# Performance work log

Measured on AMD Instinct MI355X. Metric: run time of the kernel, lower is better.

## Reference

```python
import jax, jax.numpy as jnp
import numpy as np

D_MODEL = 768
N_HEADS = 12
D_K = D_MODEL // N_HEADS
NEG = -1e9


def setup_inputs() -> dict:
    key = jax.random.key(0)
    ks = jax.random.split(key, 10)
    B, S = 2, 2048
    x = jax.random.normal(ks[0], (B, S, D_MODEL), dtype=jnp.float32)
    # causal mask, broadcastable over batch and heads
    mask = jnp.tril(jnp.ones((S, S), dtype=jnp.int32))[None, None]
    scale = 1.0 / np.sqrt(D_MODEL)
    def lin(k):
        return jax.random.normal(k, (D_MODEL, D_MODEL), dtype=jnp.float32) * scale
    return {
        "x": x, "mask": mask,
        "wq": lin(ks[1]), "bq": jnp.zeros((D_MODEL,), jnp.float32),
        "wk": lin(ks[2]), "bk": jnp.zeros((D_MODEL,), jnp.float32),
        "wv": lin(ks[3]), "bv": jnp.zeros((D_MODEL,), jnp.float32),
        "wo": lin(ks[4]), "bo": jnp.zeros((D_MODEL,), jnp.float32),
    }


def reference(x, mask, wq, bq, wk, bk, wv, bv, wo, bo):
    B, S, _ = x.shape
    def split_heads(t):  # [B,S,D] -> [B,H,S,dk]
        return t.reshape(B, S, N_HEADS, D_K).transpose(0, 2, 1, 3)
    q = split_heads(x @ wq + bq)
    k = split_heads(x @ wk + bk)
    v = split_heads(x @ wv + bv)
    scores = jnp.einsum("bhqd,bhkd->bhqk", q, k) / jnp.sqrt(jnp.float32(D_K))
    scores = jnp.where(mask == 0, NEG, scores)
    attn = jax.nn.softmax(scores, axis=-1)
    # dropout is identity in eval mode
    ctx = jnp.einsum("bhqk,bhkd->bhqd", attn, v)
    ctx = ctx.transpose(0, 2, 1, 3).reshape(B, S, D_MODEL)
    return ctx @ wo + bo
```

## Files before the change

### kernel.cpp

```cpp
#include <hip/hip_runtime.h>
#include <hip/hip_bf16.h>
#include <stdint.h>

#define DM   768
#define NH   12
#define DKH  64
#define BB   2
#define SS   2048
#define MT   (BB*SS)
#define NQKV (3*DM)

typedef __attribute__((ext_vector_type(8))) short short8;
typedef __attribute__((ext_vector_type(4))) float f32x4;

__device__ __forceinline__ unsigned short f2bf(float f) {
    union { float f; unsigned u; } v; v.f = f;
    unsigned r = v.u + 0x7fffu + ((v.u >> 16) & 1u);
    return (unsigned short)(r >> 16);
}

__device__ __forceinline__ void gload_lds16(const unsigned short* g, unsigned short* l) {
    __builtin_amdgcn_global_load_lds((const __attribute__((address_space(1))) void*)g,
                                     (__attribute__((address_space(3))) void*)l, 16, 0, 0);
}

__global__ void k_conv_x(const float* __restrict__ x, unsigned short* __restrict__ xb) {
    int i = blockIdx.x * 256 + threadIdx.x;
    const float4 v = ((const float4*)x)[i];
    ushort4 o;
    o.x = f2bf(v.x); o.y = f2bf(v.y); o.z = f2bf(v.z); o.w = f2bf(v.w);
    ((ushort4*)xb)[i] = o;
}

__global__ void k_conv_w(const float* __restrict__ wq, const float* __restrict__ wk,
                         const float* __restrict__ wv, const float* __restrict__ wo,
                         unsigned short* __restrict__ wT) {
    int idx = blockIdx.x * 256 + threadIdx.x;
    int r = idx / DM;
    int k = idx - r * DM;
    int sel = r / DM;
    int n = r - sel * DM;
    const float* w = (sel == 0) ? wq : (sel == 1) ? wk : (sel == 2) ? wv : wo;
    wT[idx] = f2bf(w[k * DM + n]);
}

__launch_bounds__(256)
__global__ void k_gemm_qkv(const unsigned short* __restrict__ xb,
                           const unsigned short* __restrict__ wT,
                           const float* __restrict__ bq, const float* __restrict__ bk,
                           const float* __restrict__ bv,
                           unsigned short* __restrict__ Qb,
                           unsigned short* __restrict__ Kb,
                           unsigned short* __restrict__ Vt) {
    __shared__ __align__(16) unsigned short As[128][32];
    __shared__ __align__(16) unsigned short Bs[128][32];
    const int t = threadIdx.x;
    const int m0 = blockIdx.x * 128;
    const int n0 = blockIdx.y * 128;
    const int wid = t >> 6, lane = t & 63, q4 = lane >> 4, l16 = lane & 15;
    const int wm = (wid >> 1) * 64, wn = (wid & 1) * 64;

    const int srow = wid * 32 + (lane >> 2);
    const int koff = (lane & 3) * 8;
    const unsigned short* AgL = xb + (size_t)(m0 + srow) * DM + koff;
    const unsigned short* AgH = AgL + (size_t)16 * DM;
    const unsigned short* BgL = wT + (size_t)(n0 + srow) * DM + koff;
    const unsigned short* BgH = BgL + (size_t)16 * DM;
    unsigned short* ldsA1 = &As[wid*32][0];
    unsigned short* ldsA2 = &As[wid*32 + 16][0];
    unsigned short* ldsB1 = &Bs[wid*32][0];
    unsigned short* ldsB2 = &Bs[wid*32 + 16][0];

    f32x4 acc[4][4];
    for (int i = 0; i < 4; i++) for (int j = 0; j < 4; j++)
        acc[i][j] = (f32x4){0.f, 0.f, 0.f, 0.f};

    for (int kt = 0; kt < DM; kt += 32) {
        gload_lds16(AgL + kt, ldsA1);
        gload_lds16(AgH + kt, ldsA2);
        gload_lds16(BgL + kt, ldsB1);
        gload_lds16(BgH + kt, ldsB2);
        __syncthreads();
        short8 af[4], bf[4];
        for (int i = 0; i < 4; i++) af[i] = *(const short8*)&As[wm + i*16 + l16][q4*8];
        for (int i = 0; i < 4; i++) bf[i] = *(const short8*)&Bs[wn + i*16 + l16][q4*8];
        for (int mi = 0; mi < 4; mi++)
            for (int ni = 0; ni < 4; ni++)
                acc[mi][ni] = __builtin_amdgcn_mfma_f32_16x16x32_bf16(af[mi], bf[ni], acc[mi][ni], 0, 0, 0);
        __syncthreads();
    }

    const int sel = n0 / DM;
    const float* bias = (sel == 0) ? bq : (sel == 1) ? bk : bv;
    for (int ni = 0; ni < 4; ni++) {
        const int col = n0 + wn + ni*16 + l16;
        const int c = col - sel * DM;
        const float bsv = bias[c];
        const int h = c >> 6, d = c & 63;
        for (int mi = 0; mi < 4; mi++) {
            for (int r = 0; r < 4; r++) {
                const int row = m0 + wm + mi*16 + q4*4 + r;
                const int b = row >> 11, s = row & 2047;
                const int bh = b * NH + h;
                float v = acc[mi][ni][r] + bsv;
                if (sel == 0) {
                    Qb[(bh*SS + s)*DKH + d] = f2bf(v * 0.125f);
                } else if (sel == 1) {
                    Kb[(bh*SS + s)*DKH + d] = f2bf(v);
                } else {
                    Vt[(bh*DKH + d)*SS + s] = f2bf(v);
                }
            }
        }
    }
}

__launch_bounds__(256)
__global__ void k_attn(const unsigned short* __restrict__ Qb,
                       const unsigned short* __restrict__ Kb,
                       const unsigned short* __restrict__ Vt,
                       unsigned short* __restrict__ ctx) {
    __shared__ __align__(16) unsigned short Ks[2][64][72];
    __shared__ __align__(16) unsigned short Vs[2][64][72];
    __shared__ __align__(16) unsigned short P[4][16][72];
    const int t = threadIdx.x;
    const int wid = t >> 6, lane = t & 63, q4 = lane >> 4, l16 = lane & 15;
    const int lin = blockIdx.x;
    const int bh = lin % (BB * NH);
    const int pair = lin / (BB * NH);
    const int b = bh / NH, h = bh - b * NH;

    const unsigned short* Qp = Qb + (size_t)bh * SS * DKH;
    const unsigned short* Kp = Kb + (size_t)bh * SS * DKH;
    const unsigned short* Vp = Vt + (size_t)bh * DKH * SS;

    const int srow = t >> 3;
    const int scol = (t & 7) * 8;

    for (int it = 0; it < 2; it++) {
        const int qblk = it ? (31 - pair) : pair;
        const int qw = qblk * 64 + wid * 16;

        short8 qf[2];
        for (int kc = 0; kc < 2; kc++)
            qf[kc] = *(const short8*)(Qp + (qw + l16)*DKH + kc*32 + q4*8);

        f32x4 accO[4];
        for (int j = 0; j < 4; j++) accO[j] = (f32x4){0.f, 0.f, 0.f, 0.f};
        float lacc[4] = {0.f, 0.f, 0.f, 0.f};

        {
            uint4 k0 = *(const uint4*)(Kp + (size_t)(srow)      * DKH + scol);
            uint4 k1 = *(const uint4*)(Kp + (size_t)(srow + 32) * DKH + scol);
            uint4 v0 = *(const uint4*)(Vp + (size_t)(srow)      * SS  + scol);
            uint4 v1 = *(const uint4*)(Vp + (size_t)(srow + 32) * SS  + scol);
            *(uint4*)&Ks[0][srow][scol]      = k0;
            *(uint4*)&Ks[0][srow + 32][scol] = k1;
            *(uint4*)&Vs[0][srow][scol]      = v0;
            *(uint4*)&Vs[0][srow + 32][scol] = v1;
        }
        __syncthreads();

        for (int kt = 0; kt <= qblk; kt++) {
            const int cb = kt & 1, nb = cb ^ 1;
            const bool hasN = (kt < qblk);
            uint4 nk0, nk1, nv0, nv1;
            if (hasN) {
                const int kn = (kt + 1) * 64;
                nk0 = *(const uint4*)(Kp + (size_t)(kn + srow)      * DKH + scol);
                nk1 = *(const uint4*)(Kp + (size_t)(kn + srow + 32) * DKH + scol);
                nv0 = *(const uint4*)(Vp + (size_t)(srow)      * SS + kn + scol);
                nv1 = *(const uint4*)(Vp + (size_t)(srow + 32) * SS + kn + scol);
            }
            short8 kf[4][2];
            #pragma unroll
            for (int ni = 0; ni < 4; ni++)
                #pragma unroll
                for (int kc = 0; kc < 2; kc++)
                    kf[ni][kc] = *(const short8*)&Ks[cb][ni*16 + l16][kc*32 + q4*8];
            f32x4 S[4];
            #pragma unroll
            for (int j = 0; j < 4; j++) S[j] = (f32x4){0.f, 0.f, 0.f, 0.f};
            #pragma unroll
            for (int ni = 0; ni < 4; ni++) {
                S[ni] = __builtin_amdgcn_mfma_f32_16x16x32_bf16(qf[0], kf[ni][0], S[ni], 0, 0, 0);
                S[ni] = __builtin_amdgcn_mfma_f32_16x16x32_bf16(qf[1], kf[ni][1], S[ni], 0, 0, 0);
            }
            if (kt == qblk) {
                #pragma unroll
                for (int ni = 0; ni < 4; ni++) {
                    const int key = kt*64 + ni*16 + l16;
                    #pragma unroll
                    for (int r = 0; r < 4; r++) {
                        const int qrow = qw + q4*4 + r;
                        float p = (key > qrow) ? 0.f : __expf(S[ni][r]);
                        lacc[r] += p;
                        P[wid][q4*4 + r][ni*16 + l16] = f2bf(p);
                    }
                }
            } else {
                #pragma unroll
                for (int ni = 0; ni < 4; ni++)
                    #pragma unroll
                    for (int r = 0; r < 4; r++) {
                        float p = __expf(S[ni][r]);
                        lacc[r] += p;
                        P[wid][q4*4 + r][ni*16 + l16] = f2bf(p);
                    }
            }
            asm volatile("s_waitcnt lgkmcnt(0)" ::: "memory");
            short8 pf[2];
            #pragma unroll
            for (int kc = 0; kc < 2; kc++)
                pf[kc] = *(const short8*)&P[wid][l16][kc*32 + q4*8];
            short8 vf[4][2];
            #pragma unroll
            for (int ndi = 0; ndi < 4; ndi++)
                #pragma unroll
                for (int kc = 0; kc < 2; kc++)
                    vf[ndi][kc] = *(const short8*)&Vs[cb][ndi*16 + l16][kc*32 + q4*8];
            #pragma unroll
            for (int ndi = 0; ndi < 4; ndi++)
                #pragma unroll
                for (int kc = 0; kc < 2; kc++)
                    accO[ndi] = __builtin_amdgcn_mfma_f32_16x16x32_bf16(pf[kc], vf[ndi][kc], accO[ndi], 0, 0, 0);
            if (hasN) {
                *(uint4*)&Ks[nb][srow][scol]      = nk0;
                *(uint4*)&Ks[nb][srow + 32][scol] = nk1;
                *(uint4*)&Vs[nb][srow][scol]      = nv0;
                *(uint4*)&Vs[nb][srow + 32][scol] = nv1;
            }
            __syncthreads();
        }

        for (int r = 0; r < 4; r++) {
            float l = lacc[r];
            for (int off = 1; off < 16; off <<= 1) l += __shfl_xor(l, off);
            const float inv = 1.0f / l;
            const int s = qw + q4*4 + r;
            for (int ni = 0; ni < 4; ni++)
                ctx[((size_t)(b*SS + s))*DM + h*64 + ni*16 + l16] = f2bf(accO[ni][r] * inv);
        }
    }
}

__launch_bounds__(256)
__global__ void k_gemm_proj(const unsigned short* __restrict__ ctx,
                            const unsigned short* __restrict__ woT,
                            const float* __restrict__ bo,
                            float* __restrict__ out) {
    __shared__ __align__(16) unsigned short As[128][32];
    __shared__ __align__(16) unsigned short Bs[64][32];
    const int t = threadIdx.x;
    const int m0 = blockIdx.x * 128;
    const int n0 = blockIdx.y * 64;
    const int wid = t >> 6, lane = t & 63, q4 = lane >> 4, l16 = lane & 15;
    const int wm = (wid >> 1) * 64, wn = (wid & 1) * 32;

    const int srowA = wid * 32 + (lane >> 2);
    const int srowB = wid * 16 + (lane >> 2);
    const int koff = (lane & 3) * 8;
    const unsigned short* AgL = ctx + (size_t)(m0 + srowA) * DM + koff;
    const unsigned short* AgH = AgL + (size_t)16 * DM;
    const unsigned short* BgL = woT + (size_t)(n0 + srowB) * DM + koff;
    unsigned short* ldsA1 = &As[wid*32][0];
    unsigned short* ldsA2 = &As[wid*32 + 16][0];
    unsigned short* ldsB1 = &Bs[wid*16][0];

    f32x4 acc[4][2];
    for (int i = 0; i < 4; i++) for (int j = 0; j < 2; j++)
        acc[i][j] = (f32x4){0.f, 0.f, 0.f, 0.f};

    for (int kt = 0; kt < DM; kt += 32) {
        gload_lds16(AgL + kt, ldsA1);
        gload_lds16(AgH + kt, ldsA2);
        gload_lds16(BgL + kt, ldsB1);
        __syncthreads();
        short8 af[4], bf[2];
        for (int i = 0; i < 4; i++) af[i] = *(const short8*)&As[wm + i*16 + l16][q4*8];
        for (int i = 0; i < 2; i++) bf[i] = *(const short8*)&Bs[wn + i*16 + l16][q4*8];
        for (int mi = 0; mi < 4; mi++)
            for (int ni = 0; ni < 2; ni++)
                acc[mi][ni] = __builtin_amdgcn_mfma_f32_16x16x32_bf16(af[mi], bf[ni], acc[mi][ni], 0, 0, 0);
        __syncthreads();
    }

    for (int ni = 0; ni < 2; ni++) {
        const int col = n0 + wn + ni*16 + l16;
        const float bsv = bo[col];
        for (int mi = 0; mi < 4; mi++) {
            for (int r = 0; r < 4; r++) {
                const int row = m0 + wm + mi*16 + q4*4 + r;
                out[(size_t)row * DM + col] = acc[mi][ni][r] + bsv;
            }
        }
    }
}

extern "C" void kernel_launch(void* const* d_in, const int* in_sizes, int n_in,
                              void* d_out, int out_size, void* d_ws, size_t ws_size,
                              hipStream_t stream) {
    const float* x  = (const float*)d_in[0];
    const float* wq = (const float*)d_in[2];
    const float* bq = (const float*)d_in[3];
    const float* wk = (const float*)d_in[4];
    const float* bk = (const float*)d_in[5];
    const float* wv = (const float*)d_in[6];
    const float* bv = (const float*)d_in[7];
    const float* wo = (const float*)d_in[8];
    const float* bo = (const float*)d_in[9];
    float* out = (float*)d_out;

    unsigned short* xb  = (unsigned short*)d_ws;
    unsigned short* wT  = xb + (size_t)MT * DM;
    unsigned short* Qb  = wT + (size_t)4 * DM * DM;
    unsigned short* Kb  = Qb + (size_t)BB * NH * SS * DKH;
    unsigned short* Vt  = Kb + (size_t)BB * NH * SS * DKH;
    unsigned short* ctx = Vt + (size_t)BB * NH * SS * DKH;

    k_conv_x<<<(MT * DM / 4) / 256, 256, 0, stream>>>(x, xb);
    k_conv_w<<<(4 * DM * DM) / 256, 256, 0, stream>>>(wq, wk, wv, wo, wT);
    dim3 g1(MT / 128, NQKV / 128);
    k_gemm_qkv<<<g1, 256, 0, stream>>>(xb, wT, bq, bk, bv, Qb, Kb, Vt);
    k_attn<<<dim3(16 * BB * NH), 256, 0, stream>>>(Qb, Kb, Vt, ctx);
    dim3 g3(MT / 128, DM / 64);
    k_gemm_proj<<<g3, 256, 0, stream>>>(ctx, wT + (size_t)3 * DM * DM, bo, out);
}
```

Measured before the change: 194.4 us.

## Tile weight transpose through LDS and restructure attention to 2 waves per q-block

The weight conversion kernel now transposes 32x32 tiles through shared memory, so both its reads and its writes are coalesced instead of strided. The attention kernel switches from 4 waves handling a paired q-block (16 rows each) to 2 waves handling one 64-row q-block (32 rows each), launched as one block per q-block with heaviest blocks scheduled first. Each K/V fragment read from LDS now feeds twice as many MFMAs, and P conversion uses packed bf16x2 intrinsics. The diagonal tile also skips the fully masked half for wave 0. The trade-offs are fewer waves per block and more blocks, plus load imbalance from launching causal-length blocks individually rather than in balanced pairs.

After: 226.3 us. 16.4% more time.

```diff
diff --git a/kernel.cpp b/kernel.cpp
--- a/kernel.cpp
+++ b/kernel.cpp
@@ -35,13 +35,18 @@
 __global__ void k_conv_w(const float* __restrict__ wq, const float* __restrict__ wk,
                          const float* __restrict__ wv, const float* __restrict__ wo,
                          unsigned short* __restrict__ wT) {
-    int idx = blockIdx.x * 256 + threadIdx.x;
-    int r = idx / DM;
-    int k = idx - r * DM;
-    int sel = r / DM;
-    int n = r - sel * DM;
+    __shared__ float tile[32][33];
+    const int sel = blockIdx.z;
     const float* w = (sel == 0) ? wq : (sel == 1) ? wk : (sel == 2) ? wv : wo;
-    wT[idx] = f2bf(w[k * DM + n]);
+    const int k0 = blockIdx.x * 32, n0 = blockIdx.y * 32;
+    const int tx = threadIdx.x, ty = threadIdx.y;
+    #pragma unroll
+    for (int j = 0; j < 4; j++)
+        tile[ty + 8*j][tx] = w[(size_t)(k0 + ty + 8*j) * DM + n0 + tx];
+    __syncthreads();
+    #pragma unroll
+    for (int j = 0; j < 4; j++)
+        wT[(size_t)(sel*DM + n0 + ty + 8*j) * DM + k0 + tx] = f2bf(tile[tx][ty + 8*j]);
 }
 
 __launch_bounds__(256)
@@ -115,131 +120,166 @@
     }
 }
 
-__launch_bounds__(256)
+__launch_bounds__(128)
 __global__ void k_attn(const unsigned short* __restrict__ Qb,
                        const unsigned short* __restrict__ Kb,
                        const unsigned short* __restrict__ Vt,
                        unsigned short* __restrict__ ctx) {
     __shared__ __align__(16) unsigned short Ks[2][64][72];
     __shared__ __align__(16) unsigned short Vs[2][64][72];
-    __shared__ __align__(16) unsigned short P[4][16][72];
+    __shared__ __align__(16) unsigned short P[2][32][68];
     const int t = threadIdx.x;
     const int wid = t >> 6, lane = t & 63, q4 = lane >> 4, l16 = lane & 15;
     const int lin = blockIdx.x;
     const int bh = lin % (BB * NH);
-    const int pair = lin / (BB * NH);
+    const int qblk = 31 - lin / (BB * NH);
     const int b = bh / NH, h = bh - b * NH;
+    const int qw = qblk * 64 + wid * 32;
 
     const unsigned short* Qp = Qb + (size_t)bh * SS * DKH;
     const unsigned short* Kp = Kb + (size_t)bh * SS * DKH;
     const unsigned short* Vp = Vt + (size_t)bh * DKH * SS;
 
-    const int srow = t >> 3;
-    const int scol = (t & 7) * 8;
-
-    for (int it = 0; it < 2; it++) {
-        const int qblk = it ? (31 - pair) : pair;
-        const int qw = qblk * 64 + wid * 16;
-
-        short8 qf[2];
+    short8 qf[2][2];
+    for (int mi = 0; mi < 2; mi++)
         for (int kc = 0; kc < 2; kc++)
-            qf[kc] = *(const short8*)(Qp + (qw + l16)*DKH + kc*32 + q4*8);
-
-        f32x4 accO[4];
-        for (int j = 0; j < 4; j++) accO[j] = (f32x4){0.f, 0.f, 0.f, 0.f};
-        float lacc[4] = {0.f, 0.f, 0.f, 0.f};
-
-        {
-            uint4 k0 = *(const uint4*)(Kp + (size_t)(srow)      * DKH + scol);
-            uint4 k1 = *(const uint4*)(Kp + (size_t)(srow + 32) * DKH + scol);
-            uint4 v0 = *(const uint4*)(Vp + (size_t)(srow)      * SS  + scol);
-            uint4 v1 = *(const uint4*)(Vp + (size_t)(srow + 32) * SS  + scol);
-            *(uint4*)&Ks[0][srow][scol]      = k0;
-            *(uint4*)&Ks[0][srow + 32][scol] = k1;
-            *(uint4*)&Vs[0][srow][scol]      = v0;
-            *(uint4*)&Vs[0][srow + 32][scol] = v1;
-        }
-        __syncthreads();
-
-        for (int kt = 0; kt <= qblk; kt++) {
-            const int cb = kt & 1, nb = cb ^ 1;
-            const bool hasN = (kt < qblk);
-            uint4 nk0, nk1, nv0, nv1;
-            if (hasN) {
-                const int kn = (kt + 1) * 64;
-                nk0 = *(const uint4*)(Kp + (size_t)(kn + srow)      * DKH + scol);
-                nk1 = *(const uint4*)(Kp + (size_t)(kn + srow + 32) * DKH + scol);
-                nv0 = *(const uint4*)(Vp + (size_t)(srow)      * SS + kn + scol);
-                nv1 = *(const uint4*)(Vp + (size_t)(srow + 32) * SS + kn + scol);
-            }
-            short8 kf[4][2];
-            #pragma unroll
-            for (int ni = 0; ni < 4; ni++)
-                #pragma unroll
-                for (int kc = 0; kc < 2; kc++)
-                    kf[ni][kc] = *(const short8*)&Ks[cb][ni*16 + l16][kc*32 + q4*8];
-            f32x4 S[4];
-            #pragma unroll
-            for (int j = 0; j < 4; j++) S[j] = (f32x4){0.f, 0.f, 0.f, 0.f};
-            #pragma unroll
-            for (int ni = 0; ni < 4; ni++) {
-                S[ni] = __builtin_amdgcn_mfma_f32_16x16x32_bf16(qf[0], kf[ni][0], S[ni], 0, 0, 0);
-                S[ni] = __builtin_amdgcn_mfma_f32_16x16x32_bf16(qf[1], kf[ni][1], S[ni], 0, 0, 0);
-            }
-            if (kt == qblk) {
+            qf[mi][kc] = *(const short8*)(Qp + (qw + mi*16 + l16)*DKH + kc*32 + q4*8);
+
+    f32x4 accO[2][4];
+    for (int i = 0; i < 2; i++) for (int j = 0; j < 4; j++)
+        accO[i][j] = (f32x4){0.f, 0.f, 0.f, 0.f};
+    float lacc[2][4];
+    for (int i = 0; i < 2; i++) for (int r = 0; r < 4; r++) lacc[i][r] = 0.f;
+
+    const int sr = t >> 3;
+    const int sc = (t & 7) * 8;
+
+    #pragma unroll
+    for (int j = 0; j < 4; j++) {
+        uint4 kv = *(const uint4*)(Kp + (size_t)(sr + 16*j) * DKH + sc);
+        uint4 vv = *(const uint4*)(Vp + (size_t)(sr + 16*j) * SS + sc);
+        *(uint4*)&Ks[0][sr + 16*j][sc] = kv;
+        *(uint4*)&Vs[0][sr + 16*j][sc] = vv;
+    }
+    __syncthreads();
+
+    for (int kt = 0; kt <= qblk; kt++) {
+        const int cb = kt & 1, nb = cb ^ 1;
+        const bool hasN = (kt < qblk);
+        uint4 nk[4], nv[4];
+        if (hasN) {
+            const int kn = (kt + 1) * 64;
+            #pragma unroll
+            for (int j = 0; j < 4; j++) {
+                nk[j] = *(const uint4*)(Kp + (size_t)(kn + sr + 16*j) * DKH + sc);
+                nv[j] = *(const uint4*)(Vp + (size_t)(sr + 16*j) * SS + kn + sc);
+            }
+        }
+        short8 kf[4][2];
+        #pragma unroll
+        for (int ni = 0; ni < 4; ni++)
+            #pragma unroll
+            for (int kc = 0; kc < 2; kc++)
+                kf[ni][kc] = *(const short8*)&Ks[cb][ni*16 + l16][kc*32 + q4*8];
+        f32x4 S[2][4];
+        #pragma unroll
+        for (int i = 0; i < 2; i++)
+            #pragma unroll
+            for (int j = 0; j < 4; j++)
+                S[i][j] = (f32x4){0.f, 0.f, 0.f, 0.f};
+        #pragma unroll
+        for (int ni = 0; ni < 4; ni++)
+            #pragma unroll
+            for (int mi = 0; mi < 2; mi++) {
+                S[mi][ni] = __builtin_amdgcn_mfma_f32_16x16x32_bf16(qf[mi][0], kf[ni][0], S[mi][ni], 0, 0, 0);
+                S[mi][ni] = __builtin_amdgcn_mfma_f32_16x16x32_bf16(qf[mi][1], kf[ni][1], S[mi][ni], 0, 0, 0);
+            }
+        if (kt == qblk) {
+            #pragma unroll
+            for (int mi = 0; mi < 2; mi++)
                 #pragma unroll
                 for (int ni = 0; ni < 4; ni++) {
-                    const int key = kt*64 + ni*16 + l16;
+                    const int pr = mi*16 + q4*4, pc = ni*16 + l16;
+                    if (wid == 0 && ni >= 2) {
+                        P[wid][pr+0][pc] = 0; P[wid][pr+1][pc] = 0;
+                        P[wid][pr+2][pc] = 0; P[wid][pr+3][pc] = 0;
+                        continue;
+                    }
+                    const int key = qblk*64 + ni*16 + l16;
+                    float p[4];
                     #pragma unroll
                     for (int r = 0; r < 4; r++) {
-                        const int qrow = qw + q4*4 + r;
-                        float p = (key > qrow) ? 0.f : __expf(S[ni][r]);
-                        lacc[r] += p;
-                        P[wid][q4*4 + r][ni*16 + l16] = f2bf(p);
+                        const int qrow = qw + mi*16 + q4*4 + r;
+                        p[r] = (key > qrow) ? 0.f : __expf(S[mi][ni][r]);
+                        lacc[mi][r] += p[r];
                     }
+                    union { __hip_bfloat162 v; unsigned u; } u01, u23;
+                    u01.v = __float22bfloat162_rn(make_float2(p[0], p[1]));
+                    u23.v = __float22bfloat162_rn(make_float2(p[2], p[3]));
+                    P[wid][pr+0][pc] = (unsigned short)(u01.u & 0xffffu);
+                    P[wid][pr+1][pc] = (unsigned short)(u01.u >> 16);
+                    P[wid][pr+2][pc] = (unsigned short)(u23.u & 0xffffu);
+                    P[wid][pr+3][pc] = (unsigned short)(u23.u >> 16);
                 }
-            } else {
+        } else {
+            #pragma unroll
+            for (int mi = 0; mi < 2; mi++)
                 #pragma unroll
-                for (int ni = 0; ni < 4; ni++)
+                for (int ni = 0; ni < 4; ni++) {
+                    float p[4];
                     #pragma unroll
                     for (int r = 0; r < 4; r++) {
-                        float p = __expf(S[ni][r]);
-                        lacc[r] += p;
-                        P[wid][q4*4 + r][ni*16 + l16] = f2bf(p);
+                        p[r] = __expf(S[mi][ni][r]);
+                        lacc[mi][r] += p[r];
                     }
-            }
-            asm volatile("s_waitcnt lgkmcnt(0)" ::: "memory");
-            short8 pf[2];
+                    union { __hip_bfloat162 v; unsigned u; } u01, u23;
+                    u01.v = __float22bfloat162_rn(make_float2(p[0], p[1]));
+                    u23.v = __float22bfloat162_rn(make_float2(p[2], p[3]));
+                    const int pr = mi*16 + q4*4, pc = ni*16 + l16;
+                    P[wid][pr+0][pc] = (unsigned short)(u01.u & 0xffffu);
+                    P[wid][pr+1][pc] = (unsigned short)(u01.u >> 16);
+                    P[wid][pr+2][pc] = (unsigned short)(u23.u & 0xffffu);
+                    P[wid][pr+3][pc] = (unsigned short)(u23.u >> 16);
+                }
+        }
+        asm volatile("s_waitcnt lgkmcnt(0)" ::: "memory");
+        short8 pf[2][2];
+        #pragma unroll
+        for (int mi = 0; mi < 2; mi++)
             #pragma unroll
             for (int kc = 0; kc < 2; kc++)
-                pf[kc] = *(const short8*)&P[wid][l16][kc*32 + q4*8];
-            short8 vf[4][2];
-            #pragma unroll
-            for (int ndi = 0; ndi < 4; ndi++)
+                pf[mi][kc] = *(const short8*)&P[wid][mi*16 + l16][kc*32 + q4*8];
+        short8 vf[4][2];
+        #pragma unroll
+        for (int ndi = 0; ndi < 4; ndi++)
+            #pragma unroll
+            for (int kc = 0; kc < 2; kc++)
+                vf[ndi][kc] = *(const short8*)&Vs[cb][ndi*16 + l16][kc*32 + q4*8];
+        #pragma unroll
+        for (int ndi = 0; ndi < 4; ndi++)
+            #pragma unroll
+            for (int kc = 0; kc < 2; kc++)
                 #pragma unroll
-                for (int kc = 0; kc < 2; kc++)
-                    vf[ndi][kc] = *(const short8*)&Vs[cb][ndi*16 + l16][kc*32 + q4*8];
-            #pragma unroll
-            for (int ndi = 0; ndi < 4; ndi++)
-                #pragma unroll
-                for (int kc = 0; kc < 2; kc++)
-                    accO[ndi] = __builtin_amdgcn_mfma_f32_16x16x32_bf16(pf[kc], vf[ndi][kc], accO[ndi], 0, 0, 0);
-            if (hasN) {
-                *(uint4*)&Ks[nb][srow][scol]      = nk0;
-                *(uint4*)&Ks[nb][srow + 32][scol] = nk1;
-                *(uint4*)&Vs[nb][srow][scol]      = nv0;
-                *(uint4*)&Vs[nb][srow + 32][scol] = nv1;
-            }
-            __syncthreads();
-        }
-
+                for (int mi = 0; mi < 2; mi++)
+                    accO[mi][ndi] = __builtin_amdgcn_mfma_f32_16x16x32_bf16(pf[mi][kc], vf[ndi][kc], accO[mi][ndi], 0, 0, 0);
+        if (hasN) {
+            #pragma unroll
+            for (int j = 0; j < 4; j++) {
+                *(uint4*)&Ks[nb][sr + 16*j][sc] = nk[j];
+                *(uint4*)&Vs[nb][sr + 16*j][sc] = nv[j];
+            }
+        }
+        __syncthreads();
+    }
+
+    for (int mi = 0; mi < 2; mi++) {
         for (int r = 0; r < 4; r++) {
-            float l = lacc[r];
+            float l = lacc[mi][r];
             for (int off = 1; off < 16; off <<= 1) l += __shfl_xor(l, off);
             const float inv = 1.0f / l;
-            const int s = qw + q4*4 + r;
+            const int s = qw + mi*16 + q4*4 + r;
             for (int ni = 0; ni < 4; ni++)
-                ctx[((size_t)(b*SS + s))*DM + h*64 + ni*16 + l16] = f2bf(accO[ni][r] * inv);
+                ctx[((size_t)(b*SS + s))*DM + h*64 + ni*16 + l16] = f2bf(accO[mi][ni][r] * inv);
         }
     }
 }
@@ -319,10 +359,10 @@
     unsigned short* ctx = Vt + (size_t)BB * NH * SS * DKH;
 
     k_conv_x<<<(MT * DM / 4) / 256, 256, 0, stream>>>(x, xb);
-    k_conv_w<<<(4 * DM * DM) / 256, 256, 0, stream>>>(wq, wk, wv, wo, wT);
+    k_conv_w<<<dim3(DM/32, DM/32, 4), dim3(32, 8), 0, stream>>>(wq, wk, wv, wo, wT);
     dim3 g1(MT / 128, NQKV / 128);
     k_gemm_qkv<<<g1, 256, 0, stream>>>(xb, wT, bq, bk, bv, Qb, Kb, Vt);
-    k_attn<<<dim3(16 * BB * NH), 256, 0, stream>>>(Qb, Kb, Vt, ctx);
+    k_attn<<<dim3(32 * BB * NH), 128, 0, stream>>>(Qb, Kb, Vt, ctx);
     dim3 g3(MT / 128, DM / 64);
     k_gemm_proj<<<g3, 256, 0, stream>>>(ctx, wT + (size_t)3 * DM * DM, bo, out);
 }
```

## Tile weight transpose through LDS, split attention into one q-block per workgroup

Applied to the files above, without the earlier changes.

The weight conversion kernel now transposes through a padded 32x33 LDS tile, so both the global reads and the global writes are coalesced. The attention kernel no longer pairs two q-blocks per workgroup. It launches one workgroup per q-block, longest blocks first, which doubles the grid size and helps balance the causal workload. On the diagonal tile, sub-tiles above the diagonal are now written as zeros without computing exp, and the P scratch padding shrinks to 68. bf16 packing now uses the hardware float2-to-bfloat2 conversion.

New measurement: 179.6 us. 7.6% less time.

```diff
diff --git a/kernel.cpp b/kernel.cpp
--- a/kernel.cpp
+++ b/kernel.cpp
@@ -35,13 +35,18 @@
 __global__ void k_conv_w(const float* __restrict__ wq, const float* __restrict__ wk,
                          const float* __restrict__ wv, const float* __restrict__ wo,
                          unsigned short* __restrict__ wT) {
-    int idx = blockIdx.x * 256 + threadIdx.x;
-    int r = idx / DM;
-    int k = idx - r * DM;
-    int sel = r / DM;
-    int n = r - sel * DM;
+    __shared__ float tile[32][33];
+    const int sel = blockIdx.z;
     const float* w = (sel == 0) ? wq : (sel == 1) ? wk : (sel == 2) ? wv : wo;
-    wT[idx] = f2bf(w[k * DM + n]);
+    const int k0 = blockIdx.x * 32, n0 = blockIdx.y * 32;
+    const int tx = threadIdx.x, ty = threadIdx.y;
+    #pragma unroll
+    for (int j = 0; j < 4; j++)
+        tile[ty + 8*j][tx] = w[(size_t)(k0 + ty + 8*j) * DM + n0 + tx];
+    __syncthreads();
+    #pragma unroll
+    for (int j = 0; j < 4; j++)
+        wT[(size_t)(sel*DM + n0 + ty + 8*j) * DM + k0 + tx] = f2bf(tile[tx][ty + 8*j]);
 }
 
 __launch_bounds__(256)
@@ -122,125 +127,151 @@
                        unsigned short* __restrict__ ctx) {
     __shared__ __align__(16) unsigned short Ks[2][64][72];
     __shared__ __align__(16) unsigned short Vs[2][64][72];
-    __shared__ __align__(16) unsigned short P[4][16][72];
+    __shared__ __align__(16) unsigned short P[4][16][68];
     const int t = threadIdx.x;
     const int wid = t >> 6, lane = t & 63, q4 = lane >> 4, l16 = lane & 15;
     const int lin = blockIdx.x;
     const int bh = lin % (BB * NH);
-    const int pair = lin / (BB * NH);
+    const int qblk = 31 - lin / (BB * NH);
     const int b = bh / NH, h = bh - b * NH;
+    const int qw = qblk * 64 + wid * 16;
 
     const unsigned short* Qp = Qb + (size_t)bh * SS * DKH;
     const unsigned short* Kp = Kb + (size_t)bh * SS * DKH;
     const unsigned short* Vp = Vt + (size_t)bh * DKH * SS;
 
-    const int srow = t >> 3;
-    const int scol = (t & 7) * 8;
-
-    for (int it = 0; it < 2; it++) {
-        const int qblk = it ? (31 - pair) : pair;
-        const int qw = qblk * 64 + wid * 16;
-
-        short8 qf[2];
-        for (int kc = 0; kc < 2; kc++)
-            qf[kc] = *(const short8*)(Qp + (qw + l16)*DKH + kc*32 + q4*8);
-
-        f32x4 accO[4];
-        for (int j = 0; j < 4; j++) accO[j] = (f32x4){0.f, 0.f, 0.f, 0.f};
-        float lacc[4] = {0.f, 0.f, 0.f, 0.f};
-
-        {
-            uint4 k0 = *(const uint4*)(Kp + (size_t)(srow)      * DKH + scol);
-            uint4 k1 = *(const uint4*)(Kp + (size_t)(srow + 32) * DKH + scol);
-            uint4 v0 = *(const uint4*)(Vp + (size_t)(srow)      * SS  + scol);
-            uint4 v1 = *(const uint4*)(Vp + (size_t)(srow + 32) * SS  + scol);
-            *(uint4*)&Ks[0][srow][scol]      = k0;
-            *(uint4*)&Ks[0][srow + 32][scol] = k1;
-            *(uint4*)&Vs[0][srow][scol]      = v0;
-            *(uint4*)&Vs[0][srow + 32][scol] = v1;
-        }
-        __syncthreads();
-
-        for (int kt = 0; kt <= qblk; kt++) {
-            const int cb = kt & 1, nb = cb ^ 1;
-            const bool hasN = (kt < qblk);
-            uint4 nk0, nk1, nv0, nv1;
-            if (hasN) {
-                const int kn = (kt + 1) * 64;
-                nk0 = *(const uint4*)(Kp + (size_t)(kn + srow)      * DKH + scol);
-                nk1 = *(const uint4*)(Kp + (size_t)(kn + srow + 32) * DKH + scol);
-                nv0 = *(const uint4*)(Vp + (size_t)(srow)      * SS + kn + scol);
-                nv1 = *(const uint4*)(Vp + (size_t)(srow + 32) * SS + kn + scol);
-            }
-            short8 kf[4][2];
-            #pragma unroll
-            for (int ni = 0; ni < 4; ni++)
-                #pragma unroll
-                for (int kc = 0; kc < 2; kc++)
-                    kf[ni][kc] = *(const short8*)&Ks[cb][ni*16 + l16][kc*32 + q4*8];
-            f32x4 S[4];
-            #pragma unroll
-            for (int j = 0; j < 4; j++) S[j] = (f32x4){0.f, 0.f, 0.f, 0.f};
+    const int sr = t >> 3;
+    const int sc = (t & 7) * 8;
+
+    short8 qf[2];
+    for (int kc = 0; kc < 2; kc++)
+        qf[kc] = *(const short8*)(Qp + (qw + l16)*DKH + kc*32 + q4*8);
+
+    f32x4 accO[4];
+    for (int j = 0; j < 4; j++) accO[j] = (f32x4){0.f, 0.f, 0.f, 0.f};
+    float lacc[4] = {0.f, 0.f, 0.f, 0.f};
+
+    {
+        uint4 k0 = *(const uint4*)(Kp + (size_t)(sr)      * DKH + sc);
+        uint4 k1 = *(const uint4*)(Kp + (size_t)(sr + 32) * DKH + sc);
+        uint4 v0 = *(const uint4*)(Vp + (size_t)(sr)      * SS  + sc);
+        uint4 v1 = *(const uint4*)(Vp + (size_t)(sr + 32) * SS  + sc);
+        *(uint4*)&Ks[0][sr][sc]      = k0;
+        *(uint4*)&Ks[0][sr + 32][sc] = k1;
+        *(uint4*)&Vs[0][sr][sc]      = v0;
+        *(uint4*)&Vs[0][sr + 32][sc] = v1;
+    }
+    __syncthreads();
+
+    for (int kt = 0; kt <= qblk; kt++) {
+        const int cb = kt & 1, nb = cb ^ 1;
+        const bool hasN = (kt < qblk);
+        uint4 nk0, nk1, nv0, nv1;
+        if (hasN) {
+            const int kn = (kt + 1) * 64;
+            nk0 = *(const uint4*)(Kp + (size_t)(kn + sr)      * DKH + sc);
+            nk1 = *(const uint4*)(Kp + (size_t)(kn + sr + 32) * DKH + sc);
+            nv0 = *(const uint4*)(Vp + (size_t)(sr)      * SS + kn + sc);
+            nv1 = *(const uint4*)(Vp + (size_t)(sr + 32) * SS + kn + sc);
+        }
+        short8 kf[4][2];
+        #pragma unroll
+        for (int ni = 0; ni < 4; ni++)
+            #pragma unroll
+            for (int kc = 0; kc < 2; kc++)
+                kf[ni][kc] = *(const short8*)&Ks[cb][ni*16 + l16][kc*32 + q4*8];
+        f32x4 S[4];
+        #pragma unroll
+        for (int j = 0; j < 4; j++) S[j] = (f32x4){0.f, 0.f, 0.f, 0.f};
+        #pragma unroll
+        for (int ni = 0; ni < 4; ni++) {
+            S[ni] = __builtin_amdgcn_mfma_f32_16x16x32_bf16(qf[0], kf[ni][0], S[ni], 0, 0, 0);
+            S[ni] = __builtin_amdgcn_mfma_f32_16x16x32_bf16(qf[1], kf[ni][1], S[ni], 0, 0, 0);
+        }
+        if (kt == qblk) {
             #pragma unroll
             for (int ni = 0; ni < 4; ni++) {
-                S[ni] = __builtin_amdgcn_mfma_f32_16x16x32_bf16(qf[0], kf[ni][0], S[ni], 0, 0, 0);
-                S[ni] = __builtin_amdgcn_mfma_f32_16x16x32_bf16(qf[1], kf[ni][1], S[ni], 0, 0, 0);
-            }
-            if (kt == qblk) {
-                #pragma unroll
-                for (int ni = 0; ni < 4; ni++) {
-                    const int key = kt*64 + ni*16 + l16;
+                const int pr = q4*4, pc = ni*16 + l16;
+                if (ni > wid) {
+                    P[wid][pr+0][pc] = 0; P[wid][pr+1][pc] = 0;
+                    P[wid][pr+2][pc] = 0; P[wid][pr+3][pc] = 0;
+                    continue;
+                }
+                float p[4];
+                if (ni == wid) {
                     #pragma unroll
                     for (int r = 0; r < 4; r++) {
                         const int qrow = qw + q4*4 + r;
-                        float p = (key > qrow) ? 0.f : __expf(S[ni][r]);
-                        lacc[r] += p;
-                        P[wid][q4*4 + r][ni*16 + l16] = f2bf(p);
+                        const int key = qblk*64 + ni*16 + l16;
+                        p[r] = (key > qrow) ? 0.f : __expf(S[ni][r]);
+                        lacc[r] += p[r];
+                    }
+                } else {
+                    #pragma unroll
+                    for (int r = 0; r < 4; r++) {
+                        p[r] = __expf(S[ni][r]);
+                        lacc[r] += p[r];
                     }
                 }
-            } else {
+                union { __hip_bfloat162 v; unsigned u; } u01, u23;
+                u01.v = __float22bfloat162_rn(make_float2(p[0], p[1]));
+                u23.v = __float22bfloat162_rn(make_float2(p[2], p[3]));
+                P[wid][pr+0][pc] = (unsigned short)(u01.u & 0xffffu);
+                P[wid][pr+1][pc] = (unsigned short)(u01.u >> 16);
+                P[wid][pr+2][pc] = (unsigned short)(u23.u & 0xffffu);
+                P[wid][pr+3][pc] = (unsigned short)(u23.u >> 16);
+            }
+        } else {
+            #pragma unroll
+            for (int ni = 0; ni < 4; ni++) {
+                float p[4];
                 #pragma unroll
-                for (int ni = 0; ni < 4; ni++)
-                    #pragma unroll
-                    for (int r = 0; r < 4; r++) {
-                        float p = __expf(S[ni][r]);
-                        lacc[r] += p;
-                        P[wid][q4*4 + r][ni*16 + l16] = f2bf(p);
-                    }
+                for (int r = 0; r < 4; r++) {
+                    p[r] = __expf(S[ni][r]);
+                    lacc[r] += p[r];
+                }
+                union { __hip_bfloat162 v; unsigned u; } u01, u23;
+                u01.v = __float22bfloat162_rn(make_float2(p[0], p[1]));
+                u23.v = __float22bfloat162_rn(make_float2(p[2], p[3]));
+                const int pr = q4*4, pc = ni*16 + l16;
+                P[wid][pr+0][pc] = (unsigned short)(u01.u & 0xffffu);
+                P[wid][pr+1][pc] = (unsigned short)(u01.u >> 16);
+                P[wid][pr+2][pc] = (unsigned short)(u23.u & 0xffffu);
+                P[wid][pr+3][pc] = (unsigned short)(u23.u >> 16);
             }
-            asm volatile("s_waitcnt lgkmcnt(0)" ::: "memory");
-            short8 pf[2];
+        }
+        asm volatile("s_waitcnt lgkmcnt(0)" ::: "memory");
+        short8 pf[2];
+        #pragma unroll
+        for (int kc = 0; kc < 2; kc++)
+            pf[kc] = *(const short8*)&P[wid][l16][kc*32 + q4*8];
+        short8 vf[4][2];
+        #pragma unroll
+        for (int ndi = 0; ndi < 4; ndi++)
             #pragma unroll
             for (int kc = 0; kc < 2; kc++)
-                pf[kc] = *(const short8*)&P[wid][l16][kc*32 + q4*8];
-            short8 vf[4][2];
-            #pragma unroll
-            for (int ndi = 0; ndi < 4; ndi++)
-                #pragma unroll
-                for (int kc = 0; kc < 2; kc++)
-                    vf[ndi][kc] = *(const short8*)&Vs[cb][ndi*16 + l16][kc*32 + q4*8];
-            #pragma unroll
-            for (int ndi = 0; ndi < 4; ndi++)
-                #pragma unroll
-                for (int kc = 0; kc < 2; kc++)
-                    accO[ndi] = __builtin_amdgcn_mfma_f32_16x16x32_bf16(pf[kc], vf[ndi][kc], accO[ndi], 0, 0, 0);
-            if (hasN) {
-                *(uint4*)&Ks[nb][srow][scol]      = nk0;
-                *(uint4*)&Ks[nb][srow + 32][scol] = nk1;
-                *(uint4*)&Vs[nb][srow][scol]      = nv0;
-                *(uint4*)&Vs[nb][srow + 32][scol] = nv1;
-            }
-            __syncthreads();
-        }
-
-        for (int r = 0; r < 4; r++) {
-            float l = lacc[r];
-            for (int off = 1; off < 16; off <<= 1) l += __shfl_xor(l, off);
-            const float inv = 1.0f / l;
-            const int s = qw + q4*4 + r;
-            for (int ni = 0; ni < 4; ni++)
-                ctx[((size_t)(b*SS + s))*DM + h*64 + ni*16 + l16] = f2bf(accO[ni][r] * inv);
-        }
+                vf[ndi][kc] = *(const short8*)&Vs[cb][ndi*16 + l16][kc*32 + q4*8];
+        #pragma unroll
+        for (int ndi = 0; ndi < 4; ndi++)
+            #pragma unroll
+            for (int kc = 0; kc < 2; kc++)
+                accO[ndi] = __builtin_amdgcn_mfma_f32_16x16x32_bf16(pf[kc], vf[ndi][kc], accO[ndi], 0, 0, 0);
+        if (hasN) {
+            *(uint4*)&Ks[nb][sr][sc]      = nk0;
+            *(uint4*)&Ks[nb][sr + 32][sc] = nk1;
+            *(uint4*)&Vs[nb][sr][sc]      = nv0;
+            *(uint4*)&Vs[nb][sr + 32][sc] = nv1;
+        }
+        __syncthreads();
+    }
+
+    for (int r = 0; r < 4; r++) {
+        float l = lacc[r];
+        for (int off = 1; off < 16; off <<= 1) l += __shfl_xor(l, off);
+        const float inv = 1.0f / l;
+        const int s = qw + q4*4 + r;
+        for (int ni = 0; ni < 4; ni++)
+            ctx[((size_t)(b*SS + s))*DM + h*64 + ni*16 + l16] = f2bf(accO[ni][r] * inv);
     }
 }
 
@@ -319,10 +350,10 @@
     unsigned short* ctx = Vt + (size_t)BB * NH * SS * DKH;
 
     k_conv_x<<<(MT * DM / 4) / 256, 256, 0, stream>>>(x, xb);
-    k_conv_w<<<(4 * DM * DM) / 256, 256, 0, stream>>>(wq, wk, wv, wo, wT);
+    k_conv_w<<<dim3(DM/32, DM/32, 4), dim3(32, 8), 0, stream>>>(wq, wk, wv, wo, wT);
     dim3 g1(MT / 128, NQKV / 128);
     k_gemm_qkv<<<g1, 256, 0, stream>>>(xb, wT, bq, bk, bv, Qb, Kb, Vt);
-    k_attn<<<dim3(16 * BB * NH), 256, 0, stream>>>(Qb, Kb, Vt, ctx);
+    k_attn<<<dim3(32 * BB * NH), 256, 0, stream>>>(Qb, Kb, Vt, ctx);
     dim3 g3(MT / 128, DM / 64);
     k_gemm_proj<<<g3, 256, 0, stream>>>(ctx, wT + (size_t)3 * DM * DM, bo, out);
 }
```
